# Performance work log

Measured on AMD Instinct MI355X. Metric: run time of the kernel, lower is better.

Reference implementation:

```python
import jax, jax.numpy as jnp
import numpy as np

B, T, D_IN, D_OUT, H = 4, 2048, 1024, 1024, 16
HD = D_OUT // H  # head_dim = 64


def setup_inputs() -> dict:
    key = jax.random.key(0)
    ks = jax.random.split(key, 6)
    s_in = 1.0 / np.sqrt(D_IN)
    s_out = 1.0 / np.sqrt(D_OUT)
    return {
        "x": jax.random.normal(ks[0], (B, T, D_IN), dtype=jnp.float32),
        "W_query": jax.random.uniform(ks[1], (D_IN, D_OUT), jnp.float32, -s_in, s_in),
        "W_key": jax.random.uniform(ks[2], (D_IN, D_OUT), jnp.float32, -s_in, s_in),
        "W_value": jax.random.uniform(ks[3], (D_IN, D_OUT), jnp.float32, -s_in, s_in),
        "W_out": jax.random.uniform(ks[4], (D_OUT, D_OUT), jnp.float32, -s_out, s_out),
        "b_out": jax.random.uniform(ks[5], (D_OUT,), jnp.float32, -s_out, s_out),
    }


def reference(x, W_query, W_key, W_value, W_out, b_out):
    # x: [B, T, D_IN]
    q = (x @ W_query).reshape(B, T, H, HD).transpose(0, 2, 1, 3)  # [B,H,T,HD]
    k = (x @ W_key).reshape(B, T, H, HD).transpose(0, 2, 1, 3)
    v = (x @ W_value).reshape(B, T, H, HD).transpose(0, 2, 1, 3)
    scores = jnp.einsum("bhqd,bhkd->bhqk", q, k)  # [B,H,T,T]
    causal = jnp.triu(jnp.ones((T, T), dtype=bool), k=1)
    scores = jnp.where(causal, -jnp.inf, scores)
    weights = jax.nn.softmax(scores / jnp.sqrt(jnp.float32(HD)), axis=-1)
    ctx = jnp.einsum("bhqk,bhkd->bhqd", weights, v)  # [B,H,T,HD]
    ctx = ctx.transpose(0, 2, 1, 3).reshape(B, T, D_OUT)
    return ctx @ W_out + b_out
```

## Files before the change

kernel.cpp:

```cpp
#include <hip/hip_runtime.h>
#include <math.h>

#define Bb   4
#define Tt   2048
#define DIN  1024
#define DOUT 1024
#define NH   16
#define HD   64

typedef __attribute__((ext_vector_type(8))) short bf16x8;
typedef __attribute__((ext_vector_type(4))) float f32x4;
typedef __attribute__((ext_vector_type(4))) short short4v;

__device__ __forceinline__ short f2bf(float f) {
  union { float f; unsigned u; } v; v.f = f;
  unsigned r = v.u + 0x7FFFu + ((v.u >> 16) & 1u);
  return (short)(r >> 16);
}

__device__ __forceinline__ unsigned pkbf(float a, float b) {
  unsigned r;
  asm("v_cvt_pk_bf16_f32 %0, %1, %2" : "=v"(r) : "v"(a), "v"(b));
  return r;
}

#define MFMA16(a, b, c) __builtin_amdgcn_mfma_f32_16x16x32_bf16((a), (b), (c), 0, 0, 0)

__device__ __forceinline__ void gload16(const short* g, short* l) {
  __builtin_amdgcn_global_load_lds(
      (const __attribute__((address_space(1))) void*)g,
      (__attribute__((address_space(3))) void*)l, 16, 0, 0);
}

__global__ __launch_bounds__(256) void cvt_x(const float* __restrict__ x,
                                             short* __restrict__ xb) {
  const int i = (blockIdx.x * 256 + threadIdx.x) * 4;
  float4 v = *(const float4*)(x + i);
  uint2 o;
  o.x = pkbf(v.x, v.y);
  o.y = pkbf(v.z, v.w);
  *(uint2*)(xb + i) = o;
}

__global__ __launch_bounds__(256) void cvt_wt(
    const float* __restrict__ W0, const float* __restrict__ W1,
    const float* __restrict__ W2, const float* __restrict__ W3,
    short* __restrict__ O0, short* __restrict__ O1,
    short* __restrict__ O2, short* __restrict__ O3) {
  const float* W = blockIdx.z == 0 ? W0 : blockIdx.z == 1 ? W1
                 : blockIdx.z == 2 ? W2 : W3;
  short* O = blockIdx.z == 0 ? O0 : blockIdx.z == 1 ? O1
           : blockIdx.z == 2 ? O2 : O3;
  __shared__ short t[64][65];
  const int n0 = blockIdx.x * 64, k0 = blockIdx.y * 64;
  const int tid = threadIdx.x;
#pragma unroll
  for (int i = 0; i < 16; ++i) {
    const int e = tid + 256 * i;
    const int k = e >> 6, n = e & 63;
    t[n][k] = f2bf(W[(size_t)(k0 + k) * DOUT + n0 + n]);
  }
  __syncthreads();
#pragma unroll
  for (int i = 0; i < 16; ++i) {
    const int e = tid + 256 * i;
    const int n = e >> 6, k = e & 63;
    O[(size_t)(n0 + n) * DIN + k0 + k] = t[n][k];
  }
}

template <bool QKV, bool F32OUT, bool BIAS>
__global__ __launch_bounds__(256) void gemm_bf16(
    const short* __restrict__ A, const short* __restrict__ Bt0,
    const float* __restrict__ bias, void* __restrict__ Cout,
    int M, int N, int K, float qsc) {
  constexpr int BM = 128, BN = 128, BK = 64;
  __shared__ __align__(16) short Asm[BM][BK];
  __shared__ __align__(16) short Bsm[BN][BK];

  const short* Bt = Bt0;
  short* Cb16 = (short*)Cout;
  float oscale = 1.0f;
  if (QKV) {
    const int z = blockIdx.z;
    Bt += (size_t)z * N * K;
    Cb16 += (size_t)z * M * N;
    if (z == 0) oscale = qsc;
  }

  const int tid = threadIdx.x;
  const int wid = tid >> 6, lane = tid & 63;
  const int lhi = lane >> 4, llo = lane & 15;
  const int bm = blockIdx.x * BM, bn = blockIdx.y * BN;
  const int wr = (wid >> 1) * 64, wc = (wid & 1) * 64;

  const int srow = lane >> 3;
  const int sca = ((lane & 7) ^ srow) * 8;

  f32x4 acc[4][4];
#pragma unroll
  for (int i = 0; i < 4; ++i)
#pragma unroll
    for (int j = 0; j < 4; ++j)
#pragma unroll
      for (int r = 0; r < 4; ++r) acc[i][j][r] = 0.0f;

  for (int k0 = 0; k0 < K; k0 += BK) {
    __syncthreads();
#pragma unroll
    for (int iss = 0; iss < 4; ++iss) {
      const int ra = wid * 32 + iss * 8 + srow;
      gload16(A + (size_t)(bm + ra) * K + k0 + sca, &Asm[wid * 32 + iss * 8][0]);
      gload16(Bt + (size_t)(bn + ra) * K + k0 + sca, &Bsm[wid * 32 + iss * 8][0]);
    }
    __syncthreads();

#pragma unroll
    for (int ks = 0; ks < 2; ++ks) {
      bf16x8 af[4], bfr[4];
#pragma unroll
      for (int i = 0; i < 4; ++i) {
        const int row = wr + i * 16 + llo;
        af[i] = *(const bf16x8*)&Asm[row][((ks * 4 + lhi) ^ (row & 7)) * 8];
      }
#pragma unroll
      for (int j = 0; j < 4; ++j) {
        const int row = wc + j * 16 + llo;
        bfr[j] = *(const bf16x8*)&Bsm[row][((ks * 4 + lhi) ^ (row & 7)) * 8];
      }
#pragma unroll
      for (int i = 0; i < 4; ++i)
#pragma unroll
        for (int j = 0; j < 4; ++j)
          acc[i][j] = MFMA16(af[i], bfr[j], acc[i][j]);
    }
  }

#pragma unroll
  for (int i = 0; i < 4; ++i)
#pragma unroll
    for (int j = 0; j < 4; ++j)
#pragma unroll
      for (int r = 0; r < 4; ++r) {
        const int row = bm + wr + i * 16 + lhi * 4 + r;
        const int col = bn + wc + j * 16 + llo;
        float v = acc[i][j][r] * oscale;
        if (BIAS) v += bias[col];
        if (F32OUT)
          ((float*)Cout)[(size_t)row * N + col] = v;
        else
          Cb16[(size_t)row * N + col] = f2bf(v);
      }
}

__global__ __launch_bounds__(512, 2) void attn_bf16(
    const short* __restrict__ Q, const short* __restrict__ K,
    const short* __restrict__ V, short* __restrict__ Ctx) {
  constexpr int LDK = 72;
  constexpr int LDV = 72;
  constexpr int LDP = 72;
  __shared__ __align__(16) short Ks[2][64][LDK];
  __shared__ __align__(16) short Vt[2][64][LDV];
  __shared__ __align__(16) short Ps[8][32][LDP];

  const int bid = blockIdx.x;
  const int qt = 7 - (bid >> 6);
  const int bh = bid & 63;
  const int b = bh >> 4, h = bh & 15;
  const int tid = threadIdx.x;
  const int wid = tid >> 6, lane = tid & 63;
  const int lhi = lane >> 4, llo = lane & 15;

  const size_t base_bt = (size_t)b * Tt;
  const int headoff = h * HD;
  const int q0 = qt * 256 + wid * 32;

  bf16x8 qf[2][2];
#pragma unroll
  for (int rb = 0; rb < 2; ++rb)
#pragma unroll
    for (int kf = 0; kf < 2; ++kf)
      qf[rb][kf] = *(const bf16x8*)&Q[(base_bt + q0 + rb * 16 + llo) * DOUT +
                                      headoff + kf * 32 + lhi * 8];

  float m_r[2] = {-1e30f, -1e30f}, l_r[2] = {0.0f, 0.0f};
  f32x4 oa[2][4];
#pragma unroll
  for (int rb = 0; rb < 2; ++rb)
#pragma unroll
    for (int j = 0; j < 4; ++j)
#pragma unroll
      for (int r = 0; r < 4; ++r) oa[rb][j][r] = 0.0f;

  const int skv = tid >> 3;
  const int sd0 = (tid & 7) * 8;
  const int sd3 = tid & 7;
  const int vpos = (((skv >> 3) ^ sd3) * 8) + (skv & 7);

  const int ktmax = qt * 4 + 3;

  {
    bf16x8 kreg = *(const bf16x8*)&K[(base_bt + skv) * DOUT + headoff + sd0];
    bf16x8 vreg = *(const bf16x8*)&V[(base_bt + skv) * DOUT + headoff + sd0];
    *(bf16x8*)&Ks[0][skv][sd0] = kreg;
#pragma unroll
    for (int e = 0; e < 8; ++e) Vt[0][sd0 + e][vpos] = vreg[e];
  }
  __syncthreads();

  for (int kt = 0; kt <= ktmax; ++kt) {
    const int cur = kt & 1;

    bf16x8 kreg, vreg;
    const bool haveNext = kt < ktmax;
    if (haveNext) {
      const size_t rbase = (base_bt + (kt + 1) * 64 + skv) * DOUT + headoff + sd0;
      kreg = *(const bf16x8*)&K[rbase];
      vreg = *(const bf16x8*)&V[rbase];
    }

    if (kt * 64 <= q0 + 31) {
      bf16x8 kf0[4], kf1[4];
#pragma unroll
      for (int j = 0; j < 4; ++j) {
        kf0[j] = *(const bf16x8*)&Ks[cur][j * 16 + llo][lhi * 8];
        kf1[j] = *(const bf16x8*)&Ks[cur][j * 16 + llo][32 + lhi * 8];
      }

#pragma unroll
      for (int rb = 0; rb < 2; ++rb) {
        f32x4 s[4];
#pragma unroll
        for (int j = 0; j < 4; ++j) {
#pragma unroll
          for (int r = 0; r < 4; ++r) s[j][r] = 0.0f;
          s[j] = MFMA16(kf0[j], qf[rb][0], s[j]);
          s[j] = MFMA16(kf1[j], qf[rb][1], s[j]);
        }
        if (kt * 64 + 63 > q0 + rb * 16) {
          const int qr = q0 + rb * 16 + llo;
#pragma unroll
          for (int j = 0; j < 4; ++j)
#pragma unroll
            for (int r = 0; r < 4; ++r)
              if (kt * 64 + j * 16 + lhi * 4 + r > qr) s[j][r] = -1e30f;
        }
        float a0 = fmaxf(fmaxf(s[0][0], s[0][1]), fmaxf(s[0][2], s[0][3]));
        float a1 = fmaxf(fmaxf(s[1][0], s[1][1]), fmaxf(s[1][2], s[1][3]));
        float a2 = fmaxf(fmaxf(s[2][0], s[2][1]), fmaxf(s[2][2], s[2][3]));
        float a3 = fmaxf(fmaxf(s[3][0], s[3][1]), fmaxf(s[3][2], s[3][3]));
        float mx = fmaxf(fmaxf(a0, a1), fmaxf(a2, a3));
        mx = fmaxf(mx, __shfl_xor(mx, 16));
        mx = fmaxf(mx, __shfl_xor(mx, 32));
        if (!__all(mx - m_r[rb] <= 8.0f)) {
          const float mnew = fmaxf(m_r[rb], mx);
          const float al = exp2f(m_r[rb] - mnew);
          m_r[rb] = mnew;
          l_r[rb] *= al;
          float alr[4];
#pragma unroll
          for (int r = 0; r < 4; ++r) alr[r] = __shfl(al, (lhi << 2) | r, 16);
#pragma unroll
          for (int j = 0; j < 4; ++j)
#pragma unroll
            for (int r = 0; r < 4; ++r) oa[rb][j][r] *= alr[r];
        }
        const float mc = m_r[rb];
#pragma unroll
        for (int j = 0; j < 4; ++j)
#pragma unroll
          for (int r = 0; r < 4; ++r) s[j][r] = exp2f(s[j][r] - mc);
        float b0 = (s[0][0] + s[0][1]) + (s[0][2] + s[0][3]);
        float b1 = (s[1][0] + s[1][1]) + (s[1][2] + s[1][3]);
        float b2 = (s[2][0] + s[2][1]) + (s[2][2] + s[2][3]);
        float b3 = (s[3][0] + s[3][1]) + (s[3][2] + s[3][3]);
        float rs = (b0 + b1) + (b2 + b3);
        rs += __shfl_xor(rs, 16);
        rs += __shfl_xor(rs, 32);
        l_r[rb] += rs;
#pragma unroll
        for (int j = 0; j < 4; ++j) {
          uint2 w;
          w.x = pkbf(s[j][0], s[j][1]);
          w.y = pkbf(s[j][2], s[j][3]);
          *(uint2*)&Ps[wid][rb * 16 + llo][j * 16 + lhi * 4] = w;
        }
      }

      bf16x8 vfr[2][4];
#pragma unroll
      for (int ks = 0; ks < 2; ++ks)
#pragma unroll
        for (int j = 0; j < 4; ++j) {
          const int d = j * 16 + llo;
          const int pos = ((lhi + 4 * ks) ^ ((d >> 3) & 7)) * 8;
          vfr[ks][j] = *(const bf16x8*)&Vt[cur][d][pos];
        }
#pragma unroll
      for (int rb = 0; rb < 2; ++rb)
#pragma unroll
        for (int ks = 0; ks < 2; ++ks) {
          bf16x8 paf = *(const bf16x8*)&Ps[wid][rb * 16 + llo][lhi * 8 + ks * 32];
#pragma unroll
          for (int j = 0; j < 4; ++j)
            oa[rb][j] = MFMA16(paf, vfr[ks][j], oa[rb][j]);
        }
    }

    if (haveNext) {
      const int nxt = cur ^ 1;
      *(bf16x8*)&Ks[nxt][skv][sd0] = kreg;
#pragma unroll
      for (int e = 0; e < 8; ++e) Vt[nxt][sd0 + e][vpos] = vreg[e];
    }
    __syncthreads();
  }

#pragma unroll
  for (int rb = 0; rb < 2; ++rb) {
    const float linv = 1.0f / l_r[rb];
    float lr[4];
#pragma unroll
    for (int r = 0; r < 4; ++r) lr[r] = __shfl(linv, (lhi << 2) | r, 16);
#pragma unroll
    for (int j = 0; j < 4; ++j)
#pragma unroll
      for (int r = 0; r < 4; ++r) {
        const int row = q0 + rb * 16 + lhi * 4 + r;
        const int col = headoff + j * 16 + llo;
        Ctx[(base_bt + row) * DOUT + col] = f2bf(oa[rb][j][r] * lr[r]);
      }
  }
}

extern "C" void kernel_launch(void* const* d_in, const int* in_sizes, int n_in,
                              void* d_out, int out_size, void* d_ws, size_t ws_size,
                              hipStream_t stream) {
  const float* x  = (const float*)d_in[0];
  const float* Wq = (const float*)d_in[1];
  const float* Wk = (const float*)d_in[2];
  const float* Wv = (const float*)d_in[3];
  const float* Wo = (const float*)d_in[4];
  const float* bo = (const float*)d_in[5];
  float* out = (float*)d_out;

  const size_t NTD = (size_t)Bb * Tt * DOUT;
  const size_t WSZ = (size_t)DIN * DOUT;
  short* xb  = (short*)d_ws;
  short* Wqt = xb + NTD;
  short* Wkt = Wqt + WSZ;
  short* Wvt = Wkt + WSZ;
  short* Wot = Wvt + WSZ;
  short* Qb  = Wot + WSZ;
  short* Kb  = Qb + NTD;
  short* Vb  = Kb + NTD;
  short* Cb  = Vb + NTD;

  const int M = Bb * Tt;
  const float qscale = 0.125f * 1.44269504089f;

  cvt_x<<<dim3(NTD / 1024), 256, 0, stream>>>(x, xb);
  cvt_wt<<<dim3(16, 16, 4), 256, 0, stream>>>(Wq, Wk, Wv, Wo, Wqt, Wkt, Wvt, Wot);

  gemm_bf16<true, false, false><<<dim3(64, 8, 3), 256, 0, stream>>>(
      xb, Wqt, nullptr, Qb, M, DOUT, DIN, qscale);

  attn_bf16<<<dim3(512), 512, 0, stream>>>(Qb, Kb, Vb, Cb);

  gemm_bf16<false, true, true><<<dim3(64, 8), 256, 0, stream>>>(
      Cb, Wot, bo, out, M, DOUT, DOUT, 1.0f);
}
```

Measured before the change: 272.4 us.

## Produce V transposed via separate GEMM and add MFMA priority hints

V is now computed as W_v^T·x^T by its own GEMM launch, so it lands in global memory already transposed ([D][B*T]). The attention kernel can then store V tiles into shared memory with one vector write instead of eight scalar swizzled stores, and read V fragments without XOR addressing. s_setprio is also raised around MFMA blocks in both the GEMM and attention kernels, and the causal-mask comparison is simplified. The cost is an extra kernel launch, a GEMM with a different grid shape, and the loss of the swizzle that avoided LDS bank conflicts when reading V.

```diff
diff --git a/kernel.cpp b/kernel.cpp
--- a/kernel.cpp
+++ b/kernel.cpp
@@ -7,6 +7,7 @@
 #define DOUT 1024
 #define NH   16
 #define HD   64
+#define BT   (Bb * Tt)
 
 typedef __attribute__((ext_vector_type(8))) short bf16x8;
 typedef __attribute__((ext_vector_type(4))) float f32x4;
@@ -128,11 +129,13 @@
         const int row = wc + j * 16 + llo;
         bfr[j] = *(const bf16x8*)&Bsm[row][((ks * 4 + lhi) ^ (row & 7)) * 8];
       }
+      __builtin_amdgcn_s_setprio(1);
 #pragma unroll
       for (int i = 0; i < 4; ++i)
 #pragma unroll
         for (int j = 0; j < 4; ++j)
           acc[i][j] = MFMA16(af[i], bfr[j], acc[i][j]);
+      __builtin_amdgcn_s_setprio(0);
     }
   }
 
@@ -155,7 +158,7 @@
 
 __global__ __launch_bounds__(512, 2) void attn_bf16(
     const short* __restrict__ Q, const short* __restrict__ K,
-    const short* __restrict__ V, short* __restrict__ Ctx) {
+    const short* __restrict__ Vt_g, short* __restrict__ Ctx) {
   constexpr int LDK = 72;
   constexpr int LDV = 72;
   constexpr int LDP = 72;
@@ -194,17 +197,19 @@
 
   const int skv = tid >> 3;
   const int sd0 = (tid & 7) * 8;
-  const int sd3 = tid & 7;
-  const int vpos = (((skv >> 3) ^ sd3) * 8) + (skv & 7);
 
   const int ktmax = qt * 4 + 3;
 
+  const short* kgp = K + (base_bt + skv) * DOUT + headoff + sd0;
+  const short* vgp = Vt_g + (size_t)(headoff + skv) * BT + base_bt + sd0;
+
   {
-    bf16x8 kreg = *(const bf16x8*)&K[(base_bt + skv) * DOUT + headoff + sd0];
-    bf16x8 vreg = *(const bf16x8*)&V[(base_bt + skv) * DOUT + headoff + sd0];
+    bf16x8 kreg = *(const bf16x8*)kgp;
+    bf16x8 vreg = *(const bf16x8*)vgp;
     *(bf16x8*)&Ks[0][skv][sd0] = kreg;
-#pragma unroll
-    for (int e = 0; e < 8; ++e) Vt[0][sd0 + e][vpos] = vreg[e];
+    *(bf16x8*)&Vt[0][skv][sd0] = vreg;
+    kgp += 64 * DOUT;
+    vgp += 64;
   }
   __syncthreads();
 
@@ -214,9 +219,10 @@
     bf16x8 kreg, vreg;
     const bool haveNext = kt < ktmax;
     if (haveNext) {
-      const size_t rbase = (base_bt + (kt + 1) * 64 + skv) * DOUT + headoff + sd0;
-      kreg = *(const bf16x8*)&K[rbase];
-      vreg = *(const bf16x8*)&V[rbase];
+      kreg = *(const bf16x8*)kgp;
+      vreg = *(const bf16x8*)vgp;
+      kgp += 64 * DOUT;
+      vgp += 64;
     }
 
     if (kt * 64 <= q0 + 31) {
@@ -230,6 +236,7 @@
 #pragma unroll
       for (int rb = 0; rb < 2; ++rb) {
         f32x4 s[4];
+        __builtin_amdgcn_s_setprio(1);
 #pragma unroll
         for (int j = 0; j < 4; ++j) {
 #pragma unroll
@@ -237,13 +244,14 @@
           s[j] = MFMA16(kf0[j], qf[rb][0], s[j]);
           s[j] = MFMA16(kf1[j], qf[rb][1], s[j]);
         }
+        __builtin_amdgcn_s_setprio(0);
         if (kt * 64 + 63 > q0 + rb * 16) {
-          const int qr = q0 + rb * 16 + llo;
+          const int kvrel = kt * 64 + lhi * 4 - (q0 + rb * 16 + llo);
 #pragma unroll
           for (int j = 0; j < 4; ++j)
 #pragma unroll
             for (int r = 0; r < 4; ++r)
-              if (kt * 64 + j * 16 + lhi * 4 + r > qr) s[j][r] = -1e30f;
+              if (kvrel + j * 16 + r > 0) s[j][r] = -1e30f;
         }
         float a0 = fmaxf(fmaxf(s[0][0], s[0][1]), fmaxf(s[0][2], s[0][3]));
         float a1 = fmaxf(fmaxf(s[1][0], s[1][1]), fmaxf(s[1][2], s[1][3]));
@@ -291,11 +299,9 @@
 #pragma unroll
       for (int ks = 0; ks < 2; ++ks)
 #pragma unroll
-        for (int j = 0; j < 4; ++j) {
-          const int d = j * 16 + llo;
-          const int pos = ((lhi + 4 * ks) ^ ((d >> 3) & 7)) * 8;
-          vfr[ks][j] = *(const bf16x8*)&Vt[cur][d][pos];
-        }
+        for (int j = 0; j < 4; ++j)
+          vfr[ks][j] = *(const bf16x8*)&Vt[cur][j * 16 + llo][ks * 32 + lhi * 8];
+      __builtin_amdgcn_s_setprio(1);
 #pragma unroll
       for (int rb = 0; rb < 2; ++rb)
 #pragma unroll
@@ -305,13 +311,13 @@
           for (int j = 0; j < 4; ++j)
             oa[rb][j] = MFMA16(paf, vfr[ks][j], oa[rb][j]);
         }
+      __builtin_amdgcn_s_setprio(0);
     }
 
     if (haveNext) {
       const int nxt = cur ^ 1;
       *(bf16x8*)&Ks[nxt][skv][sd0] = kreg;
-#pragma unroll
-      for (int e = 0; e < 8; ++e) Vt[nxt][sd0 + e][vpos] = vreg[e];
+      *(bf16x8*)&Vt[nxt][skv][sd0] = vreg;
     }
     __syncthreads();
   }
@@ -353,8 +359,8 @@
   short* Wot = Wvt + WSZ;
   short* Qb  = Wot + WSZ;
   short* Kb  = Qb + NTD;
-  short* Vb  = Kb + NTD;
-  short* Cb  = Vb + NTD;
+  short* Vtb = Kb + NTD;
+  short* Cb  = Vtb + NTD;
 
   const int M = Bb * Tt;
   const float qscale = 0.125f * 1.44269504089f;
@@ -362,10 +368,12 @@
   cvt_x<<<dim3(NTD / 1024), 256, 0, stream>>>(x, xb);
   cvt_wt<<<dim3(16, 16, 4), 256, 0, stream>>>(Wq, Wk, Wv, Wo, Wqt, Wkt, Wvt, Wot);
 
-  gemm_bf16<true, false, false><<<dim3(64, 8, 3), 256, 0, stream>>>(
+  gemm_bf16<true, false, false><<<dim3(64, 8, 2), 256, 0, stream>>>(
       xb, Wqt, nullptr, Qb, M, DOUT, DIN, qscale);
-
-  attn_bf16<<<dim3(512), 512, 0, stream>>>(Qb, Kb, Vb, Cb);
+  gemm_bf16<false, false, false><<<dim3(8, 64), 256, 0, stream>>>(
+      Wvt, xb, nullptr, Vtb, DOUT, M, DIN, 1.0f);
+
+  attn_bf16<<<dim3(512), 512, 0, stream>>>(Qb, Kb, Vtb, Cb);
 
   gemm_bf16<false, true, true><<<dim3(64, 8), 256, 0, stream>>>(
       Cb, Wot, bo, out, M, DOUT, DOUT, 1.0f);
```

New measurement: 273.2 us. About the same (+0.3%).
